# Optimization experiments

Measured on AMD Instinct MI355X. Metric: run time of the kernel, lower is better.

Reference implementation:

```python
import jax, jax.numpy as jnp
import numpy as np

B, S, D, H, E = 8, 2048, 1024, 4096, 8


def setup_inputs() -> dict:
    key = jax.random.key(0)
    k0, k1, k2, k3 = jax.random.split(key, 4)
    x = jax.random.normal(k0, (B, S, D), dtype=jnp.float32)
    # hash-router assignment: one expert per token, shape [B, S, 1] (top-k dim k=1)
    assign = jax.random.randint(k1, (B, S, 1), 0, E, dtype=jnp.int64)
    # per-expert Linear(dim, hidden): W_e [E, D, H], b_e [E, H]
    W_e = jax.random.normal(k2, (E, D, H), dtype=jnp.float32) * (1.0 / np.sqrt(D))
    b_e = jnp.zeros((E, H), dtype=jnp.float32)
    # shared output Linear(hidden, dim)
    W_out = jax.random.normal(k3, (H, D), dtype=jnp.float32) * (1.0 / np.sqrt(H))
    b_out = jnp.zeros((D,), dtype=jnp.float32)
    return {"x": x, "W_e": W_e, "b_e": b_e, "W_out": W_out, "b_out": b_out,
            "assign": assign}


def reference(x, W_e, b_e, W_out, b_out, assign):
    num_experts = W_e.shape[0]
    hidden = W_e.shape[2]
    # zero-init combine buffer, matching torch.zeros(batch, seq, hidden)
    expert_out = jnp.zeros(x.shape[:2] + (hidden,), dtype=x.dtype)
    for e in range(num_experts):  # fixed small expert loop
        y = jnp.einsum("bsd,dh->bsh", x, W_e[e]) + b_e[e]
        mask = (assign == e).any(-1)  # [B, S]
        expert_out = jnp.where(mask[..., None], y, expert_out)
    h = jax.nn.relu(expert_out)
    return jnp.einsum("bsh,hd->bsd", h, W_out) + b_out
```

## Files before the change

kernel.cpp:

```cpp
#include <hip/hip_runtime.h>
#include <hip/hip_bf16.h>
#include <stdint.h>

#define NB 8
#define NS 2048
#define ND 1024
#define NH 4096
#define NE 8
#define NTOK (NB*NS)

typedef __bf16 bf16;
typedef bf16 bf16x8 __attribute__((ext_vector_type(8)));
typedef float f32x4 __attribute__((ext_vector_type(4)));

static const size_t OFF_XB  = 128 * 1024;
static const size_t OFF_WTE = OFF_XB  + (size_t)NTOK * ND * 2;
static const size_t OFF_WTO = OFF_WTE + (size_t)NE * NH * ND * 2;
static const size_t OFF_HB  = OFF_WTO + (size_t)ND * NH * 2;
static const size_t WS_NEED = OFF_HB  + (size_t)NTOK * NH * 2;

#define GLDS16(src, dst) __builtin_amdgcn_global_load_lds( \
    (__attribute__((address_space(1))) void*)(void*)(src), \
    (__attribute__((address_space(3))) void*)(dst), 16, 0, 0)


__global__ void k_cvt_x(const float* __restrict__ in, bf16* __restrict__ out) {
    long i = (long)blockIdx.x * blockDim.x + threadIdx.x;
    const float4* in4 = (const float4*)in;
    float4 v0 = in4[i * 2];
    float4 v1 = in4[i * 2 + 1];
    bf16x8 o;
    o[0] = (bf16)v0.x; o[1] = (bf16)v0.y; o[2] = (bf16)v0.z; o[3] = (bf16)v0.w;
    o[4] = (bf16)v1.x; o[5] = (bf16)v1.y; o[6] = (bf16)v1.z; o[7] = (bf16)v1.w;
    *(bf16x8*)(out + i * 8) = o;
}

__global__ void k_hist(const int* __restrict__ assign, int* __restrict__ meta) {
    int t = blockIdx.x * blockDim.x + threadIdx.x;
    if (t < NTOK) atomicAdd(&meta[assign[t] & 7], 1);
}

__global__ void k_desc(int* __restrict__ meta) {
    if (threadIdx.x != 0 || blockIdx.x != 0) return;
    int* counts = meta;
    int* offs = meta + 16;
    offs[0] = 0;
    for (int e = 0; e < NE; e++) offs[e + 1] = offs[e] + counts[e];
    int* te  = meta + 32;
    int* trs = meta + 128;
    int* trc = meta + 256;
    int nt = 0;
    for (int e = 0; e < NE; e++) {
        int c = counts[e];
        for (int t0 = 0; t0 < c; t0 += 256) {
            te[nt] = e; trs[nt] = offs[e] + t0; trc[nt] = min(256, c - t0);
            nt++;
        }
    }
    meta[25] = nt;
}

__global__ void k_scatter(const int* __restrict__ assign, int* __restrict__ meta) {
    int t = blockIdx.x * blockDim.x + threadIdx.x;
    if (t < NTOK) {
        int e = assign[t] & 7;
        int p = atomicAdd(&meta[8 + e], 1);
        int* perm = meta + 512;
        perm[meta[16 + e] + p] = t;
    }
}

__global__ void k_transpose(const float* __restrict__ in, bf16* __restrict__ out,
                            int R, int C) {
    __shared__ float tile[32][33];
    int b  = blockIdx.z;
    int c0 = blockIdx.x * 32, r0 = blockIdx.y * 32;
    const float* inb = in + (size_t)b * R * C;
    bf16* outb = out + (size_t)b * R * C;
    int tx = threadIdx.x, ty = threadIdx.y;
#pragma unroll
    for (int i = 0; i < 4; i++) {
        int r = r0 + ty + i * 8;
        tile[ty + i * 8][tx] = inb[(size_t)r * C + c0 + tx];
    }
    __syncthreads();
#pragma unroll
    for (int i = 0; i < 4; i++) {
        int c = c0 + ty + i * 8;
        outb[(size_t)c * R + r0 + tx] = (bf16)tile[tx][ty + i * 8];
    }
}


#define BAR { __builtin_amdgcn_s_barrier(); asm volatile("" ::: "memory"); }
#define VMC4 asm volatile("s_waitcnt vmcnt(4)" ::: "memory")
#define VMC0 asm volatile("s_waitcnt vmcnt(0)" ::: "memory")

#define LDA(msub) { \
  const char* Ab = sm + dbuf + wr * 16384; \
  _Pragma("unroll") for (int m = 0; m < 4; m++) { \
    int row = ((msub) * 4 + m) * 16 + lr; \
    af[m][0] = *(const bf16x8*)(Ab + row * 128 + xk0); \
    af[m][1] = *(const bf16x8*)(Ab + row * 128 + xk1); \
  } }

#define LDB(nsub) { \
  const char* Bb = sm + dbuf + 32768 + (wc >> 1) * 16384; \
  _Pragma("unroll") for (int n = 0; n < 2; n++) { \
    int row = (wc & 1) * 64 + ((nsub) * 2 + n) * 16 + lr; \
    bfr[(nsub)*2+n][0] = *(const bf16x8*)(Bb + row * 128 + xk0); \
    bfr[(nsub)*2+n][1] = *(const bf16x8*)(Bb + row * 128 + xk1); \
  } }

#define MFMA_Q(msub, nsub) { \
  __builtin_amdgcn_s_setprio(1); \
  _Pragma("unroll") for (int m = 0; m < 4; m++) \
  _Pragma("unroll") for (int n = 0; n < 2; n++) \
  _Pragma("unroll") for (int k = 0; k < 2; k++) \
    acc[(msub)*4+m][(nsub)*2+n] = __builtin_amdgcn_mfma_f32_16x16x32_bf16( \
        af[m][k], bfr[(nsub)*2+n][k], acc[(msub)*4+m][(nsub)*2+n], 0, 0, 0); \
  __builtin_amdgcn_s_setprio(0); }

#define DO_TILE(i, S0, S1, S2, S3, VW) { \
  const int dbuf = ((i) & 1) * 65536; \
  LDA(0); LDB(0); S0; BAR; MFMA_Q(0,0); BAR; \
  LDB(1);         S1; BAR; MFMA_Q(0,1); BAR; \
  LDA(1);         S2; BAR; MFMA_Q(1,0); BAR; \
                  S3; VW; BAR; MFMA_Q(1,1); BAR; \
}

__launch_bounds__(512, 2)
__global__ void k_gemm1(const bf16* __restrict__ xb, const bf16* __restrict__ wte,
                        const float* __restrict__ b_e, bf16* __restrict__ hb,
                        const int* __restrict__ meta) {
    __shared__ __align__(16) char sm[2 * 65536];
    int nt = meta[25];
    int tileIdx = blockIdx.y;
    if (tileIdx >= nt) return;
    int e  = meta[32 + tileIdx];
    int rs = meta[128 + tileIdx];
    int rc = meta[256 + tileIdx];
    const int* perm = meta + 512;
    int n0 = blockIdx.x * 256;

    int tid = threadIdx.x;
    int lane = tid & 63, wid = tid >> 6;
    int wr = wid >> 2, wc = wid & 3;
    int lr = lane & 15, kg = lane >> 4;
    int xk0 = (kg ^ (lr & 7)) * 16;
    int xk1 = ((4 + kg) ^ (lr & 7)) * 16;

    int sr = tid >> 3, sl = tid & 7;
    int g = sl ^ (sr & 7);
    const bf16* pa[2][2];
#pragma unroll
    for (int h = 0; h < 2; h++)
#pragma unroll
      for (int r = 0; r < 2; r++) {
        int arow = h * 128 + r * 64 + sr;
        int tok = perm[rs + (arow < rc - 1 ? arow : rc - 1)];
        pa[h][r] = xb + (size_t)tok * ND + g * 8;
      }
    const bf16* pb0 = wte + ((size_t)e * NH + n0 + sr) * ND + g * 8;

#define STAGE_A(t, h) { \
    char* d = sm + ((t) & 1) * 65536 + (h) * 16384 + wid * 1024; \
    GLDS16(pa[h][0] + (size_t)(t) * 64, d); \
    GLDS16(pa[h][1] + (size_t)(t) * 64, d + 8192); }
#define STAGE_B(t, h) { \
    char* d = sm + ((t) & 1) * 65536 + 32768 + (h) * 16384 + wid * 1024; \
    GLDS16(pb0 + ((h) * 128) * (size_t)ND + (size_t)(t) * 64, d); \
    GLDS16(pb0 + ((h) * 128 + 64) * (size_t)ND + (size_t)(t) * 64, d + 8192); }

    f32x4 acc[8][4] = {};
    bf16x8 af[4][2], bfr[4][2];
    const int NT = ND / 64;

    STAGE_B(0, 0); STAGE_B(0, 1); STAGE_A(0, 0); STAGE_A(0, 1);
    STAGE_B(1, 0); STAGE_B(1, 1);
    VMC4;
    BAR;

#pragma unroll 2
    for (int i = 0; i < NT - 2; i++)
        DO_TILE(i, STAGE_A(i + 1, 0), STAGE_A(i + 1, 1),
                   STAGE_B(i + 2, 0), STAGE_B(i + 2, 1), VMC4);
    DO_TILE(NT - 2, STAGE_A(NT - 1, 0), STAGE_A(NT - 1, 1), , , VMC0);
    DO_TILE(NT - 1, , , , , );

    float bias[4];
#pragma unroll
    for (int n = 0; n < 4; n++) bias[n] = b_e[e * NH + n0 + wc * 64 + n * 16 + lr];
#pragma unroll
    for (int m = 0; m < 8; m++) {
#pragma unroll
        for (int r = 0; r < 4; r++) {
            int row = wr * 128 + m * 16 + kg * 4 + r;
            if (row < rc) {
                bf16* hp = hb + (size_t)(rs + row) * NH + n0 + wc * 64;
#pragma unroll
                for (int n = 0; n < 4; n++)
                    hp[n * 16 + lr] = (bf16)fmaxf(acc[m][n][r] + bias[n], 0.0f);
            }
        }
    }
#undef STAGE_A
#undef STAGE_B
}

__launch_bounds__(512, 2)
__global__ void k_gemm2(const bf16* __restrict__ hb, const bf16* __restrict__ wto,
                        const float* __restrict__ b_out, const int* __restrict__ meta,
                        float* __restrict__ out) {
    __shared__ __align__(16) char sm[2 * 65536];
    int lin = blockIdx.x;
    int swz = (lin & 7) * 32 + (lin >> 3);
    int bx = swz & 3, by = swz >> 2;
    int m0 = by * 256, n0 = bx * 256;
    const int* perm = meta + 512;

    int tid = threadIdx.x;
    int lane = tid & 63, wid = tid >> 6;
    int wr = wid >> 2, wc = wid & 3;
    int lr = lane & 15, kg = lane >> 4;
    int xk0 = (kg ^ (lr & 7)) * 16;
    int xk1 = ((4 + kg) ^ (lr & 7)) * 16;

    int sr = tid >> 3, sl = tid & 7;
    int g = sl ^ (sr & 7);
    const bf16* pa0 = hb  + ((size_t)m0 + sr) * NH + g * 8;
    const bf16* pb0 = wto + ((size_t)n0 + sr) * NH + g * 8;

#define STAGE_A(t, h) { \
    char* d = sm + ((t) & 1) * 65536 + (h) * 16384 + wid * 1024; \
    GLDS16(pa0 + ((h) * 128) * (size_t)NH + (size_t)(t) * 64, d); \
    GLDS16(pa0 + ((h) * 128 + 64) * (size_t)NH + (size_t)(t) * 64, d + 8192); }
#define STAGE_B(t, h) { \
    char* d = sm + ((t) & 1) * 65536 + 32768 + (h) * 16384 + wid * 1024; \
    GLDS16(pb0 + ((h) * 128) * (size_t)NH + (size_t)(t) * 64, d); \
    GLDS16(pb0 + ((h) * 128 + 64) * (size_t)NH + (size_t)(t) * 64, d + 8192); }

    f32x4 acc[8][4] = {};
    bf16x8 af[4][2], bfr[4][2];
    const int NT = NH / 64;

    STAGE_B(0, 0); STAGE_B(0, 1); STAGE_A(0, 0); STAGE_A(0, 1);
    STAGE_B(1, 0); STAGE_B(1, 1);
    VMC4;
    BAR;

#pragma unroll 2
    for (int i = 0; i < NT - 2; i++)
        DO_TILE(i, STAGE_A(i + 1, 0), STAGE_A(i + 1, 1),
                   STAGE_B(i + 2, 0), STAGE_B(i + 2, 1), VMC4);
    DO_TILE(NT - 2, STAGE_A(NT - 1, 0), STAGE_A(NT - 1, 1), , , VMC0);
    DO_TILE(NT - 1, , , , , );

    float bias[4];
#pragma unroll
    for (int n = 0; n < 4; n++) bias[n] = b_out[n0 + wc * 64 + n * 16 + lr];
#pragma unroll
    for (int m = 0; m < 8; m++) {
#pragma unroll
        for (int r = 0; r < 4; r++) {
            int prow = m0 + wr * 128 + m * 16 + kg * 4 + r;
            int tok = perm[prow];
            float* op = out + (size_t)tok * ND + n0 + wc * 64;
#pragma unroll
            for (int n = 0; n < 4; n++)
                op[n * 16 + lr] = acc[m][n][r] + bias[n];
        }
    }
#undef STAGE_A
#undef STAGE_B
}

extern "C" void kernel_launch(void* const* d_in, const int* in_sizes, int n_in,
                              void* d_out, int out_size, void* d_ws, size_t ws_size,
                              hipStream_t stream) {
    const float* x     = (const float*)d_in[0];
    const float* W_e   = (const float*)d_in[1];
    const float* b_e   = (const float*)d_in[2];
    const float* W_out = (const float*)d_in[3];
    const float* b_out = (const float*)d_in[4];
    const int*   assign = (const int*)d_in[5];
    float* out = (float*)d_out;

    if (ws_size < WS_NEED) return;

    char* ws = (char*)d_ws;
    int*  meta = (int*)ws;
    bf16* xb  = (bf16*)(ws + OFF_XB);
    bf16* wte = (bf16*)(ws + OFF_WTE);
    bf16* wto = (bf16*)(ws + OFF_WTO);
    bf16* hb  = (bf16*)(ws + OFF_HB);

    hipMemsetAsync(meta, 0, 512 * sizeof(int), stream);

    k_cvt_x<<<NTOK * ND / (256 * 8), 256, 0, stream>>>(x, xb);
    k_hist<<<NTOK / 256, 256, 0, stream>>>(assign, meta);
    k_desc<<<1, 64, 0, stream>>>(meta);
    k_scatter<<<NTOK / 256, 256, 0, stream>>>(assign, meta);
    k_transpose<<<dim3(NH / 32, ND / 32, NE), dim3(32, 8), 0, stream>>>(W_e, wte, ND, NH);
    k_transpose<<<dim3(ND / 32, NH / 32, 1), dim3(32, 8), 0, stream>>>(W_out, wto, NH, ND);
    k_gemm1<<<dim3(NH / 256, 72), 512, 0, stream>>>(xb, wte, b_e, hb, meta);
    k_gemm2<<<256, 512, 0, stream>>>(hb, wto, b_out, meta, out);
}
```

Measured before the change: 493.0 us.

## Gather-convert x into expert-sorted order and remap gemm1 tiles per XCD

Replaces the plain x conversion with a gather-convert kernel that writes bf16 rows already permuted into expert-sorted order. gemm1 can then read contiguous rows instead of indirect per-token rows. gemm1 uses a 1D grid whose block index is decoded so tiles of the same row block land on the same XCD, which should improve L2 reuse of A. k_desc is also parallelized across lanes. The risk is that the gather step reads x with scattered row accesses.

```diff
diff --git a/kernel.cpp b/kernel.cpp
--- a/kernel.cpp
+++ b/kernel.cpp
@@ -24,40 +24,32 @@
     (__attribute__((address_space(3))) void*)(dst), 16, 0, 0)
 
 
-__global__ void k_cvt_x(const float* __restrict__ in, bf16* __restrict__ out) {
-    long i = (long)blockIdx.x * blockDim.x + threadIdx.x;
-    const float4* in4 = (const float4*)in;
-    float4 v0 = in4[i * 2];
-    float4 v1 = in4[i * 2 + 1];
-    bf16x8 o;
-    o[0] = (bf16)v0.x; o[1] = (bf16)v0.y; o[2] = (bf16)v0.z; o[3] = (bf16)v0.w;
-    o[4] = (bf16)v1.x; o[5] = (bf16)v1.y; o[6] = (bf16)v1.z; o[7] = (bf16)v1.w;
-    *(bf16x8*)(out + i * 8) = o;
-}
-
 __global__ void k_hist(const int* __restrict__ assign, int* __restrict__ meta) {
     int t = blockIdx.x * blockDim.x + threadIdx.x;
     if (t < NTOK) atomicAdd(&meta[assign[t] & 7], 1);
 }
 
 __global__ void k_desc(int* __restrict__ meta) {
-    if (threadIdx.x != 0 || blockIdx.x != 0) return;
-    int* counts = meta;
-    int* offs = meta + 16;
+    int lane = threadIdx.x;
+    int counts[NE], offs[NE + 1];
     offs[0] = 0;
-    for (int e = 0; e < NE; e++) offs[e + 1] = offs[e] + counts[e];
-    int* te  = meta + 32;
-    int* trs = meta + 128;
-    int* trc = meta + 256;
+#pragma unroll
+    for (int e = 0; e < NE; e++) { counts[e] = meta[e]; offs[e + 1] = offs[e] + counts[e]; }
+    if (lane < NE + 1) meta[16 + lane] = offs[lane];
+    int base[NE];
     int nt = 0;
-    for (int e = 0; e < NE; e++) {
-        int c = counts[e];
-        for (int t0 = 0; t0 < c; t0 += 256) {
-            te[nt] = e; trs[nt] = offs[e] + t0; trc[nt] = min(256, c - t0);
-            nt++;
-        }
-    }
-    meta[25] = nt;
+#pragma unroll
+    for (int e = 0; e < NE; e++) { base[e] = nt; nt += (counts[e] + 255) >> 8; }
+    if (lane == 0) meta[25] = nt;
+    for (int t = lane; t < nt; t += 64) {
+        int e = 0;
+#pragma unroll
+        for (int k = 1; k < NE; k++) if (t >= base[k]) e = k;
+        int t0 = (t - base[e]) << 8;
+        meta[32 + t] = e;
+        meta[128 + t] = offs[e] + t0;
+        meta[256 + t] = min(256, counts[e] - t0);
+    }
 }
 
 __global__ void k_scatter(const int* __restrict__ assign, int* __restrict__ meta) {
@@ -68,6 +60,21 @@
         int* perm = meta + 512;
         perm[meta[16 + e] + p] = t;
     }
+}
+
+__global__ void k_gather_cvt(const float* __restrict__ x, const int* __restrict__ meta,
+                             bf16* __restrict__ xbp) {
+    long i = (long)blockIdx.x * blockDim.x + threadIdx.x;
+    int row = (int)(i >> 7);
+    int c8  = (int)(i & 127);
+    const int* perm = meta + 512;
+    int tok = perm[row];
+    const float4* s = (const float4*)(x + (size_t)tok * ND + c8 * 8);
+    float4 v0 = s[0], v1 = s[1];
+    bf16x8 o;
+    o[0] = (bf16)v0.x; o[1] = (bf16)v0.y; o[2] = (bf16)v0.z; o[3] = (bf16)v0.w;
+    o[4] = (bf16)v1.x; o[5] = (bf16)v1.y; o[6] = (bf16)v1.z; o[7] = (bf16)v1.w;
+    *(bf16x8*)(xbp + i * 8) = o;
 }
 
 __global__ void k_transpose(const float* __restrict__ in, bf16* __restrict__ out,
@@ -130,18 +137,20 @@
 }
 
 __launch_bounds__(512, 2)
-__global__ void k_gemm1(const bf16* __restrict__ xb, const bf16* __restrict__ wte,
+__global__ void k_gemm1(const bf16* __restrict__ xbp, const bf16* __restrict__ wte,
                         const float* __restrict__ b_e, bf16* __restrict__ hb,
                         const int* __restrict__ meta) {
     __shared__ __align__(16) char sm[2 * 65536];
     int nt = meta[25];
-    int tileIdx = blockIdx.y;
+    int f = blockIdx.x;
+    int xcd = f & 7, j = f >> 3;
+    int bx = j & 15, tslot = j >> 4;
+    int tileIdx = xcd + 8 * tslot;
     if (tileIdx >= nt) return;
     int e  = meta[32 + tileIdx];
     int rs = meta[128 + tileIdx];
     int rc = meta[256 + tileIdx];
-    const int* perm = meta + 512;
-    int n0 = blockIdx.x * 256;
+    int n0 = bx * 256;
 
     int tid = threadIdx.x;
     int lane = tid & 63, wid = tid >> 6;
@@ -158,8 +167,8 @@
 #pragma unroll
       for (int r = 0; r < 2; r++) {
         int arow = h * 128 + r * 64 + sr;
-        int tok = perm[rs + (arow < rc - 1 ? arow : rc - 1)];
-        pa[h][r] = xb + (size_t)tok * ND + g * 8;
+        int p = rs + (arow < rc - 1 ? arow : rc - 1);
+        pa[h][r] = xbp + (size_t)p * ND + g * 8;
       }
     const bf16* pb0 = wte + ((size_t)e * NH + n0 + sr) * ND + g * 8;
 
@@ -290,19 +299,19 @@
 
     char* ws = (char*)d_ws;
     int*  meta = (int*)ws;
-    bf16* xb  = (bf16*)(ws + OFF_XB);
+    bf16* xbp = (bf16*)(ws + OFF_XB);
     bf16* wte = (bf16*)(ws + OFF_WTE);
     bf16* wto = (bf16*)(ws + OFF_WTO);
     bf16* hb  = (bf16*)(ws + OFF_HB);
 
     hipMemsetAsync(meta, 0, 512 * sizeof(int), stream);
 
-    k_cvt_x<<<NTOK * ND / (256 * 8), 256, 0, stream>>>(x, xb);
     k_hist<<<NTOK / 256, 256, 0, stream>>>(assign, meta);
     k_desc<<<1, 64, 0, stream>>>(meta);
     k_scatter<<<NTOK / 256, 256, 0, stream>>>(assign, meta);
+    k_gather_cvt<<<NTOK * ND / (256 * 8), 256, 0, stream>>>(x, meta, xbp);
     k_transpose<<<dim3(NH / 32, ND / 32, NE), dim3(32, 8), 0, stream>>>(W_e, wte, ND, NH);
     k_transpose<<<dim3(ND / 32, NH / 32, 1), dim3(32, 8), 0, stream>>>(W_out, wto, NH, ND);
-    k_gemm1<<<dim3(NH / 256, 72), 512, 0, stream>>>(xb, wte, b_e, hb, meta);
+    k_gemm1<<<1152, 512, 0, stream>>>(xbp, wte, b_e, hb, meta);
     k_gemm2<<<256, 512, 0, stream>>>(hb, wto, b_out, meta, out);
 }
```

Result: no change. 490.9 us (-0.4%).
